# Performance work log

Measured on AMD Instinct MI355X. Metric: run time of the kernel, lower is better.

## Reference

```python
import jax, jax.numpy as jnp
import numpy as np

DT = 0.01
GAMMA = 1.0
EPSILON = 1.0
DIFFUSIVE_GAMMA = 0.0


def setup_inputs() -> dict:
    key = jax.random.key(0)
    k1, k2, k3, k4 = jax.random.split(key, 4)
    B, T, n_inp, n_hid = 128, 1024, 64, 512
    x = jax.random.normal(k1, (B, T, n_inp), dtype=jnp.float32)
    x2h = jax.random.uniform(k2, (n_inp, n_hid), dtype=jnp.float32)
    h2h = jax.random.normal(k3, (n_hid, n_hid), dtype=jnp.float32) / jnp.sqrt(jnp.float32(n_hid))
    bias = jax.random.uniform(k4, (n_hid,), dtype=jnp.float32) * 2.0 - 1.0
    return {"x": x, "x2h": x2h, "h2h": h2h, "bias": bias}


def reference(x, x2h, h2h, bias):
    # x: [B, T, n_inp]
    B, T, _ = x.shape
    n_hid = h2h.shape[0]
    w = h2h - DIFFUSIVE_GAMMA * jnp.eye(n_hid, dtype=h2h.dtype)  # loop-invariant
    wT = w.T
    i2h_all = jnp.tanh(jnp.einsum('bti,ih->bth', x, x2h))  # precompute input path

    def step(carry, i2h_t):
        hy, hz = carry
        rec = jnp.tanh(hy @ w + bias) @ wT  # [B, n_hid]
        hz = hz + DT * (i2h_t - rec - GAMMA * hy - EPSILON * hz)
        hy = hy + DT * hz
        return (hy, hz), hy

    hy0 = jnp.zeros((B, n_hid), dtype=x.dtype)
    hz0 = jnp.zeros((B, n_hid), dtype=x.dtype)
    (hy_f, hz_f), states = jax.lax.scan(step, (hy0, hz0), jnp.swapaxes(i2h_all, 0, 1))
    all_states = jnp.swapaxes(states, 0, 1)  # [B, T, n_hid]
    return all_states, hy_f
```

## Files before the change

### kernel.cpp

```cpp
#include <hip/hip_runtime.h>

#define DT 0.01f
#define NH 512
#define T_STEPS 1024
#define NB 128
#define SLICE 64
#define SCALE_F 262144.0f
#define INV_SCALE 3.814697265625e-6f

typedef _Float16 h2v __attribute__((ext_vector_type(2)));
typedef _Float16 h8v __attribute__((ext_vector_type(8)));

#if defined(__has_builtin)
#if __has_builtin(__builtin_amdgcn_fdot2)
#define HAVE_FDOT2 1
#endif
#endif

#ifdef HAVE_FDOT2
#define FDOT2(a, b, c) __builtin_amdgcn_fdot2((a), (b), (c), false)
#else
static __device__ __forceinline__ float FDOT2(h2v a, h2v b, float c) {
    return c + (float)a[0] * (float)b[0] + (float)a[1] * (float)b[1];
}
#endif

#define O_W1 0
#define O_W2 65536
#define O_HY 131072
#define O_S  135168
#define LDS_BYTES 135680

__global__ __launch_bounds__(512) void i2h_kernel(const float* __restrict__ x,
                                                  const float* __restrict__ x2h,
                                                  float* __restrict__ out) {
    __shared__ __align__(16) float xs[16 * 64];
    int bt0 = blockIdx.x * 16;
    int tid = threadIdx.x;
    xs[tid]       = x[(size_t)bt0 * 64 + tid];
    xs[tid + 512] = x[(size_t)bt0 * 64 + tid + 512];
    __syncthreads();

    float acc[16];
    #pragma unroll
    for (int r = 0; r < 16; ++r) acc[r] = 0.f;

    for (int i4 = 0; i4 < 16; ++i4) {
        float w0 = x2h[(i4 * 4 + 0) * 512 + tid];
        float w1 = x2h[(i4 * 4 + 1) * 512 + tid];
        float w2 = x2h[(i4 * 4 + 2) * 512 + tid];
        float w3 = x2h[(i4 * 4 + 3) * 512 + tid];
        #pragma unroll
        for (int r = 0; r < 16; ++r) {
            float4 xv = *(const float4*)&xs[r * 64 + i4 * 4];
            acc[r] += xv.x * w0 + xv.y * w1 + xv.z * w2 + xv.w * w3;
        }
    }
    #pragma unroll
    for (int r = 0; r < 16; ++r)
        out[(size_t)(bt0 + r) * 512 + tid] = tanhf(acc[r]);
}

__global__ __launch_bounds__(512, 1) void recur5(const float* __restrict__ h2h,
                                                 const float* __restrict__ bias,
                                                 float* __restrict__ out,
                                                 unsigned long long* __restrict__ recbuf) {
    extern __shared__ unsigned char lds[];
    h8v* w1p      = (h8v*)(lds + O_W1);
    h8v* w2p      = (h8v*)(lds + O_W2);
    _Float16* hyH = (_Float16*)(lds + O_HY);
    _Float16* stg = (_Float16*)(lds + O_S);

    const int tid = threadIdx.x;
    const int m   = blockIdx.x >> 5;
    const int G   = blockIdx.x & 31;
    const int jm  = m * SLICE;
    const int p   = tid;

    const int w    = tid >> 6;
    const int r1   = w >> 1;
    const int jj1  = (w & 1) * 32 + (tid & 31);
    const int half = (tid >> 5) & 1;

    for (int it = 0; it < 8; ++it) {
        int gidx = it * 512 + tid;
        int i8 = gidx >> 6, j = gidx & 63;
        h8v wv;
        #pragma unroll
        for (int e = 0; e < 8; ++e)
            wv[e] = (_Float16)h2h[(size_t)(i8 * 8 + e) * NH + jm + j];
        w1p[i8 * 64 + j] = wv;
    }
    for (int it = 0; it < 8; ++it) {
        int gidx = it * 512 + tid;
        int pr = gidx >> 3, k = gidx & 7;
        const float* rp = h2h + (size_t)pr * NH + jm + k * 8;
        h8v wv;
        #pragma unroll
        for (int e = 0; e < 8; ++e) wv[e] = (_Float16)rp[e];
        w2p[pr * 8 + (k ^ (pr & 7))] = wv;
    }

    #pragma unroll
    for (int r = 0; r < 4; ++r) hyH[r * NH + p] = (_Float16)0.f;

    unsigned long long* rb = recbuf + (size_t)G * 2048;

    const float bj1 = bias[jm + jj1];

    const float* ivBase = out + (size_t)(4 * G) * T_STEPS * NH + p;
    float* outBase      = out + (size_t)(4 * G) * T_STEPS * NH + p;
    const bool writer = ((p >> 6) == m);

    float hy[4] = {0.f, 0.f, 0.f, 0.f};
    float hz[4] = {0.f, 0.f, 0.f, 0.f};
    int pvA[4] = {0, 0, 0, 0};
    int pvB[4] = {0, 0, 0, 0};

    float iv[4];
    #pragma unroll
    for (int r = 0; r < 4; ++r) iv[r] = ivBase[(size_t)r * T_STEPS * NH];

    __syncthreads();

    for (int t = 0; t < T_STEPS; ++t) {
        float ivn[4] = {0.f, 0.f, 0.f, 0.f};
        if (t + 1 < T_STEPS) {
            #pragma unroll
            for (int r = 0; r < 4; ++r)
                ivn[r] = ivBase[((size_t)r * T_STEPS + (t + 1)) * NH];
        }

        {
            float acc = 0.f;
            const _Float16* hyRow = hyH + r1 * NH + half * 256;
            const h8v* wBase = w1p + (half * 32) * 64 + jj1;
            #pragma unroll 8
            for (int kk = 0; kk < 32; ++kk) {
                h8v wv = wBase[kk * 64];
                h8v av = *(const h8v*)(hyRow + kk * 8);
                h2v wA = {wv[0], wv[1]}, wB = {wv[2], wv[3]},
                    wC = {wv[4], wv[5]}, wD = {wv[6], wv[7]};
                h2v aA = {av[0], av[1]}, aB = {av[2], av[3]},
                    aC = {av[4], av[5]}, aD = {av[6], av[7]};
                acc = FDOT2(wA, aA, acc); acc = FDOT2(wB, aB, acc);
                acc = FDOT2(wC, aC, acc); acc = FDOT2(wD, aD, acc);
            }
            float tot = acc + __shfl_xor(acc, 32);
            float sv = tanhf(tot + bj1);
            if (half == 0) stg[r1 * 64 + jj1] = (_Float16)sv;
        }
        __syncthreads();

        float acc[4] = {0.f, 0.f, 0.f, 0.f};
        {
            const int sw = p & 7;
            #pragma unroll
            for (int k = 0; k < 8; ++k) {
                h8v wv = w2p[p * 8 + (k ^ sw)];
                h2v wA = {wv[0], wv[1]}, wB = {wv[2], wv[3]},
                    wC = {wv[4], wv[5]}, wD = {wv[6], wv[7]};
                #pragma unroll
                for (int r = 0; r < 4; ++r) {
                    h8v sv = *(const h8v*)(stg + r * 64 + k * 8);
                    h2v sA = {sv[0], sv[1]}, sB = {sv[2], sv[3]},
                        sC = {sv[4], sv[5]}, sD = {sv[6], sv[7]};
                    float a = acc[r];
                    a = FDOT2(wA, sA, a); a = FDOT2(wB, sB, a);
                    a = FDOT2(wC, sC, a); a = FDOT2(wD, sD, a);
                    acc[r] = a;
                }
            }
        }

        int q0 = (int)rintf(acc[0] * SCALE_F);
        int q1 = (int)rintf(acc[1] * SCALE_F);
        int q2 = (int)rintf(acc[2] * SCALE_F);
        int q3 = (int)rintf(acc[3] * SCALE_F);
        int dA0, dB0, dA1, dB1;
        if (t & 1) {
            dA0 = q0 - pvB[0]; pvB[0] = q0;  dB0 = q1 - pvB[1]; pvB[1] = q1;
            dA1 = q2 - pvB[2]; pvB[2] = q2;  dB1 = q3 - pvB[3]; pvB[3] = q3;
        } else {
            dA0 = q0 - pvA[0]; pvA[0] = q0;  dB0 = q1 - pvA[1]; pvA[1] = q1;
            dA1 = q2 - pvA[2]; pvA[2] = q2;  dB1 = q3 - pvA[3]; pvA[3] = q3;
        }
        unsigned long long c0 =
            (1ull << 50) + (unsigned long long)(((long long)dA0 << 25) + (long long)dB0);
        unsigned long long c1 =
            (1ull << 50) + (unsigned long long)(((long long)dA1 << 25) + (long long)dB1);

        const int par = t & 1;
        unsigned long long* e0 = rb + par * 1024 + p;
        unsigned long long* e1 = e0 + 512;

        asm volatile("s_waitcnt vmcnt(0)" ::: "memory");
        __hip_atomic_fetch_add(e0, c0, __ATOMIC_RELAXED, __HIP_MEMORY_SCOPE_AGENT);
        __hip_atomic_fetch_add(e1, c1, __ATOMIC_RELAXED, __HIP_MEMORY_SCOPE_AGENT);

        const long long expc = 8ll * (long long)((t >> 1) + 1);
        long long S0 = 0, S1 = 0, S2 = 0, S3 = 0;
        bool d0 = false, d1 = false;
        for (;;) {
            unsigned long long v0 = 0, v1 = 0;
            if (!d0) v0 = __hip_atomic_load(e0, __ATOMIC_RELAXED, __HIP_MEMORY_SCOPE_AGENT);
            if (!d1) v1 = __hip_atomic_load(e1, __ATOMIC_RELAXED, __HIP_MEMORY_SCOPE_AGENT);
            if (!d0) {
                long long sB = ((long long)(v0 << 39)) >> 39;
                unsigned long long v2 = v0 - (unsigned long long)sB;
                long long sA = ((long long)(v2 << 14)) >> 39;
                long long cnt = (long long)((v2 - ((unsigned long long)sA << 25)) >> 50);
                if (cnt >= expc) { S0 = sA; S1 = sB; d0 = true; }
            }
            if (!d1) {
                long long sB = ((long long)(v1 << 39)) >> 39;
                unsigned long long v2 = v1 - (unsigned long long)sB;
                long long sA = ((long long)(v2 << 14)) >> 39;
                long long cnt = (long long)((v2 - ((unsigned long long)sA << 25)) >> 50);
                if (cnt >= expc) { S2 = sA; S3 = sB; d1 = true; }
            }
            if (d0 && d1) break;
            __builtin_amdgcn_s_sleep(1);
        }

        float rec[4] = {(float)S0 * INV_SCALE, (float)S1 * INV_SCALE,
                        (float)S2 * INV_SCALE, (float)S3 * INV_SCALE};
        #pragma unroll
        for (int r = 0; r < 4; ++r) {
            hz[r] = hz[r] + DT * (iv[r] - rec[r] - hy[r] - hz[r]);
            hy[r] = hy[r] + DT * hz[r];
            hyH[r * NH + p] = (_Float16)hy[r];
        }
        if (writer) {
            #pragma unroll
            for (int r = 0; r < 4; ++r)
                outBase[((size_t)r * T_STEPS + t) * NH] = hy[r];
        }
        #pragma unroll
        for (int r = 0; r < 4; ++r) iv[r] = ivn[r];
        __syncthreads();
    }

    if (writer) {
        #pragma unroll
        for (int r = 0; r < 4; ++r)
            out[(size_t)NB * T_STEPS * NH + (size_t)(4 * G + r) * NH + p] = hy[r];
    }
}

extern "C" void kernel_launch(void* const* d_in, const int* in_sizes, int n_in,
                              void* d_out, int out_size, void* d_ws, size_t ws_size,
                              hipStream_t stream) {
    const float* x    = (const float*)d_in[0];
    const float* x2h  = (const float*)d_in[1];
    const float* h2h  = (const float*)d_in[2];
    const float* bias = (const float*)d_in[3];
    float* out = (float*)d_out;

    unsigned long long* recbuf = (unsigned long long*)d_ws;

    hipMemsetAsync(d_ws, 0, 32 * 2048 * sizeof(unsigned long long), stream);

    i2h_kernel<<<8192, 512, 0, stream>>>(x, x2h, out);

    hipFuncSetAttribute((const void*)recur5,
                        hipFuncAttributeMaxDynamicSharedMemorySize, LDS_BYTES);
    recur5<<<256, 512, LDS_BYTES, stream>>>(h2h, bias, out, recbuf);
}
```

Measured before the change: 4.384 ms.

## Replace packed atomic-add reduction with per-block slots and flag barrier

Replaces the cross-block reduction, which used fixed-point quantized deltas packed into 64-bit atomic adds with per-thread polling, with plain fp32 partial stores into per-block slots. Each block then raises a release flag, and the eight blocks of a group spin on each other's flags before reading and summing the eight partials. Also caches the first-stage fp16 weights in registers instead of re-reading LDS each step. This removes atomic contention and polling traffic but adds two block-wide syncs per step and more register pressure.

Result: slower. 9.238 ms (+110.7%).

```diff
diff --git a/kernel.cpp b/kernel.cpp
--- a/kernel.cpp
+++ b/kernel.cpp
@@ -5,8 +5,6 @@
 #define T_STEPS 1024
 #define NB 128
 #define SLICE 64
-#define SCALE_F 262144.0f
-#define INV_SCALE 3.814697265625e-6f
 
 typedef _Float16 h2v __attribute__((ext_vector_type(2)));
 typedef _Float16 h8v __attribute__((ext_vector_type(8)));
@@ -24,6 +22,15 @@
     return c + (float)a[0] * (float)b[0] + (float)a[1] * (float)b[1];
 }
 #endif
+
+static __device__ __forceinline__ unsigned long long pack2f(float a, float b) {
+    union { float f[2]; unsigned long long u; } x;
+    x.f[0] = a; x.f[1] = b; return x.u;
+}
+static __device__ __forceinline__ void unpack2f(unsigned long long u, float& a, float& b) {
+    union { unsigned long long u; float f[2]; } x;
+    x.u = u; a = x.f[0]; b = x.f[1];
+}
 
 #define O_W1 0
 #define O_W2 65536
@@ -61,10 +68,11 @@
         out[(size_t)(bt0 + r) * 512 + tid] = tanhf(acc[r]);
 }
 
-__global__ __launch_bounds__(512, 1) void recur5(const float* __restrict__ h2h,
+__global__ __launch_bounds__(512, 1) void recur6(const float* __restrict__ h2h,
                                                  const float* __restrict__ bias,
                                                  float* __restrict__ out,
-                                                 unsigned long long* __restrict__ recbuf) {
+                                                 unsigned long long* __restrict__ recbuf,
+                                                 unsigned int* __restrict__ flags) {
     extern __shared__ unsigned char lds[];
     h8v* w1p      = (h8v*)(lds + O_W1);
     h8v* w2p      = (h8v*)(lds + O_W2);
@@ -104,7 +112,15 @@
     #pragma unroll
     for (int r = 0; r < 4; ++r) hyH[r * NH + p] = (_Float16)0.f;
 
-    unsigned long long* rb = recbuf + (size_t)G * 2048;
+    __syncthreads();
+
+    h8v w1r[32];
+    #pragma unroll
+    for (int kk = 0; kk < 32; ++kk)
+        w1r[kk] = w1p[(half * 32 + kk) * 64 + jj1];
+
+    unsigned long long* rb = recbuf + (size_t)G * 16384;
+    unsigned int* flagBase = flags + G * 128;
 
     const float bj1 = bias[jm + jj1];
 
@@ -114,14 +130,10 @@
 
     float hy[4] = {0.f, 0.f, 0.f, 0.f};
     float hz[4] = {0.f, 0.f, 0.f, 0.f};
-    int pvA[4] = {0, 0, 0, 0};
-    int pvB[4] = {0, 0, 0, 0};
 
     float iv[4];
     #pragma unroll
     for (int r = 0; r < 4; ++r) iv[r] = ivBase[(size_t)r * T_STEPS * NH];
-
-    __syncthreads();
 
     for (int t = 0; t < T_STEPS; ++t) {
         float ivn[4] = {0.f, 0.f, 0.f, 0.f};
@@ -134,10 +146,9 @@
         {
             float acc = 0.f;
             const _Float16* hyRow = hyH + r1 * NH + half * 256;
-            const h8v* wBase = w1p + (half * 32) * 64 + jj1;
-            #pragma unroll 8
+            #pragma unroll
             for (int kk = 0; kk < 32; ++kk) {
-                h8v wv = wBase[kk * 64];
+                h8v wv = w1r[kk];
                 h8v av = *(const h8v*)(hyRow + kk * 8);
                 h2v wA = {wv[0], wv[1]}, wB = {wv[2], wv[3]},
                     wC = {wv[4], wv[5]}, wD = {wv[6], wv[7]};
@@ -173,63 +184,47 @@
             }
         }
 
-        int q0 = (int)rintf(acc[0] * SCALE_F);
-        int q1 = (int)rintf(acc[1] * SCALE_F);
-        int q2 = (int)rintf(acc[2] * SCALE_F);
-        int q3 = (int)rintf(acc[3] * SCALE_F);
-        int dA0, dB0, dA1, dB1;
-        if (t & 1) {
-            dA0 = q0 - pvB[0]; pvB[0] = q0;  dB0 = q1 - pvB[1]; pvB[1] = q1;
-            dA1 = q2 - pvB[2]; pvB[2] = q2;  dB1 = q3 - pvB[3]; pvB[3] = q3;
-        } else {
-            dA0 = q0 - pvA[0]; pvA[0] = q0;  dB0 = q1 - pvA[1]; pvA[1] = q1;
-            dA1 = q2 - pvA[2]; pvA[2] = q2;  dB1 = q3 - pvA[3]; pvA[3] = q3;
-        }
-        unsigned long long c0 =
-            (1ull << 50) + (unsigned long long)(((long long)dA0 << 25) + (long long)dB0);
-        unsigned long long c1 =
-            (1ull << 50) + (unsigned long long)(((long long)dA1 << 25) + (long long)dB1);
-
         const int par = t & 1;
-        unsigned long long* e0 = rb + par * 1024 + p;
-        unsigned long long* e1 = e0 + 512;
-
-        asm volatile("s_waitcnt vmcnt(0)" ::: "memory");
-        __hip_atomic_fetch_add(e0, c0, __ATOMIC_RELAXED, __HIP_MEMORY_SCOPE_AGENT);
-        __hip_atomic_fetch_add(e1, c1, __ATOMIC_RELAXED, __HIP_MEMORY_SCOPE_AGENT);
-
-        const long long expc = 8ll * (long long)((t >> 1) + 1);
-        long long S0 = 0, S1 = 0, S2 = 0, S3 = 0;
-        bool d0 = false, d1 = false;
-        for (;;) {
-            unsigned long long v0 = 0, v1 = 0;
-            if (!d0) v0 = __hip_atomic_load(e0, __ATOMIC_RELAXED, __HIP_MEMORY_SCOPE_AGENT);
-            if (!d1) v1 = __hip_atomic_load(e1, __ATOMIC_RELAXED, __HIP_MEMORY_SCOPE_AGENT);
-            if (!d0) {
-                long long sB = ((long long)(v0 << 39)) >> 39;
-                unsigned long long v2 = v0 - (unsigned long long)sB;
-                long long sA = ((long long)(v2 << 14)) >> 39;
-                long long cnt = (long long)((v2 - ((unsigned long long)sA << 25)) >> 50);
-                if (cnt >= expc) { S0 = sA; S1 = sB; d0 = true; }
-            }
-            if (!d1) {
-                long long sB = ((long long)(v1 << 39)) >> 39;
-                unsigned long long v2 = v1 - (unsigned long long)sB;
-                long long sA = ((long long)(v2 << 14)) >> 39;
-                long long cnt = (long long)((v2 - ((unsigned long long)sA << 25)) >> 50);
-                if (cnt >= expc) { S2 = sA; S3 = sB; d1 = true; }
-            }
-            if (d0 && d1) break;
-            __builtin_amdgcn_s_sleep(1);
-        }
-
-        float rec[4] = {(float)S0 * INV_SCALE, (float)S1 * INV_SCALE,
-                        (float)S2 * INV_SCALE, (float)S3 * INV_SCALE};
+        unsigned long long* myslot = rb + par * 8192 + m * 1024 + p;
+        __hip_atomic_store(myslot, pack2f(acc[0], acc[1]),
+                           __ATOMIC_RELAXED, __HIP_MEMORY_SCOPE_AGENT);
+        __hip_atomic_store(myslot + 512, pack2f(acc[2], acc[3]),
+                           __ATOMIC_RELAXED, __HIP_MEMORY_SCOPE_AGENT);
+
+        __syncthreads();
+        if (tid == 0)
+            __hip_atomic_store(flagBase + m * 16, (unsigned int)(t + 1),
+                               __ATOMIC_RELEASE, __HIP_MEMORY_SCOPE_AGENT);
+        if (tid < 8) {
+            const unsigned int* fp = flagBase + tid * 16;
+            while (__hip_atomic_load(fp, __ATOMIC_ACQUIRE, __HIP_MEMORY_SCOPE_AGENT)
+                   <= (unsigned int)t)
+                __builtin_amdgcn_s_sleep(1);
+        }
+        __syncthreads();
+
+        const unsigned long long* lbase = rb + par * 8192 + p;
+        unsigned long long va[8], vb[8];
+        #pragma unroll
+        for (int mm = 0; mm < 8; ++mm) {
+            va[mm] = __hip_atomic_load(lbase + mm * 1024, __ATOMIC_RELAXED,
+                                       __HIP_MEMORY_SCOPE_AGENT);
+            vb[mm] = __hip_atomic_load(lbase + mm * 1024 + 512, __ATOMIC_RELAXED,
+                                       __HIP_MEMORY_SCOPE_AGENT);
+        }
+        float rec0 = 0.f, rec1 = 0.f, rec2 = 0.f, rec3 = 0.f;
+        #pragma unroll
+        for (int mm = 0; mm < 8; ++mm) {
+            float a, b;
+            unpack2f(va[mm], a, b); rec0 += a; rec1 += b;
+            unpack2f(vb[mm], a, b); rec2 += a; rec3 += b;
+        }
+
+        float rec[4] = {rec0, rec1, rec2, rec3};
         #pragma unroll
         for (int r = 0; r < 4; ++r) {
             hz[r] = hz[r] + DT * (iv[r] - rec[r] - hy[r] - hz[r]);
             hy[r] = hy[r] + DT * hz[r];
-            hyH[r * NH + p] = (_Float16)hy[r];
         }
         if (writer) {
             #pragma unroll
@@ -237,7 +232,10 @@
                 outBase[((size_t)r * T_STEPS + t) * NH] = hy[r];
         }
         #pragma unroll
-        for (int r = 0; r < 4; ++r) iv[r] = ivn[r];
+        for (int r = 0; r < 4; ++r) {
+            hyH[r * NH + p] = (_Float16)hy[r];
+            iv[r] = ivn[r];
+        }
         __syncthreads();
     }
 
@@ -257,13 +255,14 @@
     const float* bias = (const float*)d_in[3];
     float* out = (float*)d_out;
 
-    unsigned long long* recbuf = (unsigned long long*)d_ws;
-
-    hipMemsetAsync(d_ws, 0, 32 * 2048 * sizeof(unsigned long long), stream);
+    unsigned int* flags        = (unsigned int*)d_ws;
+    unsigned long long* recbuf = (unsigned long long*)((char*)d_ws + 65536);
+
+    hipMemsetAsync(d_ws, 0, 65536, stream);
 
     i2h_kernel<<<8192, 512, 0, stream>>>(x, x2h, out);
 
-    hipFuncSetAttribute((const void*)recur5,
+    hipFuncSetAttribute((const void*)recur6,
                         hipFuncAttributeMaxDynamicSharedMemorySize, LDS_BYTES);
-    recur5<<<256, 512, LDS_BYTES, stream>>>(h2h, bias, out, recbuf);
-}
+    recur6<<<256, 512, LDS_BYTES, stream>>>(h2h, bias, out, recbuf, flags);
+}
```

## Bias-encode packed atomic partials, interleave slots, defer output stores past atomics

Applied to the files above, without the earlier changes.

Each quantized partial sum now gets a constant offset, so the packed 64-bit atomic accumulator fields stay non-negative and can be decoded with plain masks and shifts. That makes the per-iteration spin-wait check just the two count fields. The two accumulator words per thread are placed next to each other so they share cache lines. The global store of hy is delayed by one step so it issues after the atomics and overlaps the wait, and an initial sleep is added before polling. The scale is halved to leave headroom for the offset, which lowers the fixed-point precision of the cross-block reduction.

After: 8.059 ms. 83.8% more time.

```diff
diff --git a/kernel.cpp b/kernel.cpp
--- a/kernel.cpp
+++ b/kernel.cpp
@@ -5,8 +5,10 @@
 #define T_STEPS 1024
 #define NB 128
 #define SLICE 64
-#define SCALE_F 262144.0f
-#define INV_SCALE 3.814697265625e-6f
+#define SCALE_F 131072.0f
+#define INV_SCALE 7.62939453125e-6f
+#define BIGC (1 << 21)
+#define BIAS8 (8 << 21)
 
 typedef _Float16 h2v __attribute__((ext_vector_type(2)));
 typedef _Float16 h8v __attribute__((ext_vector_type(8)));
@@ -61,7 +63,7 @@
         out[(size_t)(bt0 + r) * 512 + tid] = tanhf(acc[r]);
 }
 
-__global__ __launch_bounds__(512, 1) void recur5(const float* __restrict__ h2h,
+__global__ __launch_bounds__(512, 1) void recur7(const float* __restrict__ h2h,
                                                  const float* __restrict__ bias,
                                                  float* __restrict__ out,
                                                  unsigned long long* __restrict__ recbuf) {
@@ -114,6 +116,7 @@
 
     float hy[4] = {0.f, 0.f, 0.f, 0.f};
     float hz[4] = {0.f, 0.f, 0.f, 0.f};
+    float hyPrev[4] = {0.f, 0.f, 0.f, 0.f};
     int pvA[4] = {0, 0, 0, 0};
     int pvB[4] = {0, 0, 0, 0};
 
@@ -173,78 +176,71 @@
             }
         }
 
-        int q0 = (int)rintf(acc[0] * SCALE_F);
-        int q1 = (int)rintf(acc[1] * SCALE_F);
-        int q2 = (int)rintf(acc[2] * SCALE_F);
-        int q3 = (int)rintf(acc[3] * SCALE_F);
-        int dA0, dB0, dA1, dB1;
+        int Q0 = (int)rintf(acc[0] * SCALE_F) + BIGC;
+        int Q1 = (int)rintf(acc[1] * SCALE_F) + BIGC;
+        int Q2 = (int)rintf(acc[2] * SCALE_F) + BIGC;
+        int Q3 = (int)rintf(acc[3] * SCALE_F) + BIGC;
+        int d0, d1, d2, d3;
         if (t & 1) {
-            dA0 = q0 - pvB[0]; pvB[0] = q0;  dB0 = q1 - pvB[1]; pvB[1] = q1;
-            dA1 = q2 - pvB[2]; pvB[2] = q2;  dB1 = q3 - pvB[3]; pvB[3] = q3;
+            d0 = Q0 - pvB[0]; pvB[0] = Q0;  d1 = Q1 - pvB[1]; pvB[1] = Q1;
+            d2 = Q2 - pvB[2]; pvB[2] = Q2;  d3 = Q3 - pvB[3]; pvB[3] = Q3;
         } else {
-            dA0 = q0 - pvA[0]; pvA[0] = q0;  dB0 = q1 - pvA[1]; pvA[1] = q1;
-            dA1 = q2 - pvA[2]; pvA[2] = q2;  dB1 = q3 - pvA[3]; pvA[3] = q3;
-        }
-        unsigned long long c0 =
-            (1ull << 50) + (unsigned long long)(((long long)dA0 << 25) + (long long)dB0);
-        unsigned long long c1 =
-            (1ull << 50) + (unsigned long long)(((long long)dA1 << 25) + (long long)dB1);
+            d0 = Q0 - pvA[0]; pvA[0] = Q0;  d1 = Q1 - pvA[1]; pvA[1] = Q1;
+            d2 = Q2 - pvA[2]; pvA[2] = Q2;  d3 = Q3 - pvA[3]; pvA[3] = Q3;
+        }
+        unsigned long long c0 = (1ull << 50)
+            + ((unsigned long long)(long long)d0 << 25) + (unsigned long long)(long long)d1;
+        unsigned long long c1 = (1ull << 50)
+            + ((unsigned long long)(long long)d2 << 25) + (unsigned long long)(long long)d3;
 
         const int par = t & 1;
-        unsigned long long* e0 = rb + par * 1024 + p;
-        unsigned long long* e1 = e0 + 512;
+        unsigned long long* e0 = rb + par * 1024 + p * 2;
+        unsigned long long* e1 = e0 + 1;
 
         asm volatile("s_waitcnt vmcnt(0)" ::: "memory");
         __hip_atomic_fetch_add(e0, c0, __ATOMIC_RELAXED, __HIP_MEMORY_SCOPE_AGENT);
         __hip_atomic_fetch_add(e1, c1, __ATOMIC_RELAXED, __HIP_MEMORY_SCOPE_AGENT);
 
-        const long long expc = 8ll * (long long)((t >> 1) + 1);
-        long long S0 = 0, S1 = 0, S2 = 0, S3 = 0;
-        bool d0 = false, d1 = false;
+        if (writer && t > 0) {
+            #pragma unroll
+            for (int r = 0; r < 4; ++r)
+                outBase[((size_t)r * T_STEPS + (t - 1)) * NH] = hyPrev[r];
+        }
+
+        const unsigned int expc = 8u * (unsigned int)((t >> 1) + 1);
+        unsigned long long v0, v1;
+        __builtin_amdgcn_s_sleep(2);
         for (;;) {
-            unsigned long long v0 = 0, v1 = 0;
-            if (!d0) v0 = __hip_atomic_load(e0, __ATOMIC_RELAXED, __HIP_MEMORY_SCOPE_AGENT);
-            if (!d1) v1 = __hip_atomic_load(e1, __ATOMIC_RELAXED, __HIP_MEMORY_SCOPE_AGENT);
-            if (!d0) {
-                long long sB = ((long long)(v0 << 39)) >> 39;
-                unsigned long long v2 = v0 - (unsigned long long)sB;
-                long long sA = ((long long)(v2 << 14)) >> 39;
-                long long cnt = (long long)((v2 - ((unsigned long long)sA << 25)) >> 50);
-                if (cnt >= expc) { S0 = sA; S1 = sB; d0 = true; }
-            }
-            if (!d1) {
-                long long sB = ((long long)(v1 << 39)) >> 39;
-                unsigned long long v2 = v1 - (unsigned long long)sB;
-                long long sA = ((long long)(v2 << 14)) >> 39;
-                long long cnt = (long long)((v2 - ((unsigned long long)sA << 25)) >> 50);
-                if (cnt >= expc) { S2 = sA; S3 = sB; d1 = true; }
-            }
-            if (d0 && d1) break;
+            v0 = __hip_atomic_load(e0, __ATOMIC_RELAXED, __HIP_MEMORY_SCOPE_AGENT);
+            v1 = __hip_atomic_load(e1, __ATOMIC_RELAXED, __HIP_MEMORY_SCOPE_AGENT);
+            if ((unsigned int)(v0 >> 50) >= expc && (unsigned int)(v1 >> 50) >= expc) break;
             __builtin_amdgcn_s_sleep(1);
         }
 
-        float rec[4] = {(float)S0 * INV_SCALE, (float)S1 * INV_SCALE,
-                        (float)S2 * INV_SCALE, (float)S3 * INV_SCALE};
+        float rec[4];
+        rec[0] = (float)((int)((v0 >> 25) & 0x1FFFFFFull) - BIAS8) * INV_SCALE;
+        rec[1] = (float)((int)(v0 & 0x1FFFFFFull) - BIAS8) * INV_SCALE;
+        rec[2] = (float)((int)((v1 >> 25) & 0x1FFFFFFull) - BIAS8) * INV_SCALE;
+        rec[3] = (float)((int)(v1 & 0x1FFFFFFull) - BIAS8) * INV_SCALE;
+
         #pragma unroll
         for (int r = 0; r < 4; ++r) {
             hz[r] = hz[r] + DT * (iv[r] - rec[r] - hy[r] - hz[r]);
             hy[r] = hy[r] + DT * hz[r];
             hyH[r * NH + p] = (_Float16)hy[r];
-        }
-        if (writer) {
-            #pragma unroll
-            for (int r = 0; r < 4; ++r)
-                outBase[((size_t)r * T_STEPS + t) * NH] = hy[r];
-        }
-        #pragma unroll
-        for (int r = 0; r < 4; ++r) iv[r] = ivn[r];
+            hyPrev[r] = hy[r];
+            iv[r] = ivn[r];
+        }
         __syncthreads();
     }
 
     if (writer) {
         #pragma unroll
         for (int r = 0; r < 4; ++r)
-            out[(size_t)NB * T_STEPS * NH + (size_t)(4 * G + r) * NH + p] = hy[r];
+            outBase[((size_t)r * T_STEPS + (T_STEPS - 1)) * NH] = hyPrev[r];
+        #pragma unroll
+        for (int r = 0; r < 4; ++r)
+            out[(size_t)NB * T_STEPS * NH + (size_t)(4 * G + r) * NH + p] = hyPrev[r];
     }
 }
 
@@ -263,7 +259,7 @@
 
     i2h_kernel<<<8192, 512, 0, stream>>>(x, x2h, out);
 
-    hipFuncSetAttribute((const void*)recur5,
+    hipFuncSetAttribute((const void*)recur7,
                         hipFuncAttributeMaxDynamicSharedMemorySize, LDS_BYTES);
-    recur5<<<256, 512, LDS_BYTES, stream>>>(h2h, bias, out, recbuf);
-}
+    recur7<<<256, 512, LDS_BYTES, stream>>>(h2h, bias, out, recbuf);
+}
```
